# Optimization experiments

Measured on AMD Instinct MI355X. Metric: run time of the kernel, lower is better.

## Reference

```python
import jax, jax.numpy as jnp
import numpy as np

LOG2E = 1.4426950408889634
NUM_HEADS = 12

def fake_quant_sym8(x):
    # per-tensor symmetric int8 fake-quant (QuantStub with MovingAverageMinMax,
    # symmetric, qint8 [-128,127]); dynamic scale from current amax, STE.
    scale = jnp.maximum(jnp.max(jnp.abs(x)) / 127.0, 1e-8)
    q = jnp.clip(jnp.round(x / scale), -128.0, 127.0) * scale
    return x + jax.lax.stop_gradient(q - x)

def integer_approx_softmax(x):
    # ITA-style integer-approximated softmax: exp(x) = 2^(x*log2e),
    # split into integer/fractional parts, 2^f approximated piecewise-linearly
    # as (1 + f) for f in [0,1) (hardware shift-add friendly), then normalize.
    z = x * LOG2E
    z = z - jnp.max(z, axis=-1, keepdims=True)  # z <= 0, numerically stable
    zi = jnp.floor(z)
    zf = z - zi
    p = jnp.exp2(zi) * (1.0 + zf)
    return p / jnp.sum(p, axis=-1, keepdims=True)

def setup_inputs() -> dict:
    key = jax.random.key(0)
    ks = jax.random.split(key, 5)
    B, N, E, P = 8, 1024, 768, 768
    s = 0.02  # typical init scale for linear weights
    return {
        "x":  jax.random.normal(ks[0], (B, N, E), jnp.float32),
        "Wq": jax.random.normal(ks[1], (E, P), jnp.float32) * s,
        "bq": jnp.zeros((P,), jnp.float32),
        "Wk": jax.random.normal(ks[2], (E, P), jnp.float32) * s,
        "bk": jnp.zeros((P,), jnp.float32),
        "Wv": jax.random.normal(ks[3], (E, P), jnp.float32) * s,
        "bv": jnp.zeros((P,), jnp.float32),
        "Wo": jax.random.normal(ks[4], (P, E), jnp.float32) * s,
        "bo": jnp.zeros((E,), jnp.float32),
    }

def reference(x, Wq, bq, Wk, bk, Wv, bv, Wo, bo):
    B, N, E = x.shape
    H = NUM_HEADS
    D = Wq.shape[1] // H  # head_dim = proj_dim // num_heads
    xq = fake_quant_sym8(x)
    # projections -> [B, H, N, D]
    Q = (xq @ Wq + bq).reshape(B, N, H, D).transpose(0, 2, 1, 3)
    K = (xq @ Wk + bk).reshape(B, N, H, D).transpose(0, 2, 1, 3)
    V = (xq @ Wv + bv).reshape(B, N, H, D).transpose(0, 2, 1, 3)
    # NOTE: no 1/sqrt(D) scaling -- the torch module applies none (ITA absorbs
    # scaling into the quantization parameters).
    logits = jnp.einsum('bhnd,bhmd->bhnm', Q, K)
    attn = integer_approx_softmax(logits)
    ctx = jnp.einsum('bhnm,bhmd->bhnd', attn, V)
    ctx = ctx.transpose(0, 2, 1, 3).reshape(B, N, H * D)
    return ctx @ Wo + bo
```

## Files before the change

kernel.cpp:

```cpp
#include <hip/hip_runtime.h>


typedef unsigned short u16;
typedef __attribute__((ext_vector_type(8))) short short8;
typedef __attribute__((ext_vector_type(8))) _Float16 half8;
typedef __attribute__((ext_vector_type(4))) float f32x4;

#define LOG2E_F 1.4426950408889634f

static __device__ __forceinline__ half8 s2h(short8 s) {
  union { short8 s; half8 h; } u; u.s = s; return u.h;
}
static __device__ __forceinline__ f32x4 mfma16(short8 a, short8 b, f32x4 c) {
  return __builtin_amdgcn_mfma_f32_16x16x32_f16(s2h(a), s2h(b), c, 0, 0, 0);
}
static __device__ __forceinline__ u16 f2h(float f) {
  union { _Float16 h; u16 u; } v; v.h = (_Float16)f; return v.u;
}
static __device__ __forceinline__ void gload16(const void* g, void* l) {
  __builtin_amdgcn_global_load_lds(
      (const __attribute__((address_space(1))) void*)g,
      (__attribute__((address_space(3))) void*)l, 16, 0, 0);
}

__global__ __launch_bounds__(256) void amax_part_kernel(
    const float4* __restrict__ x, float* __restrict__ part, int n4) {
  float m = 0.f;
  int i = blockIdx.x * 256 + threadIdx.x;
  const int stride = gridDim.x * 256;
  for (; i < n4; i += stride) {
    float4 v = x[i];
    m = fmaxf(m, fmaxf(fmaxf(fabsf(v.x), fabsf(v.y)),
                       fmaxf(fabsf(v.z), fabsf(v.w))));
  }
  #pragma unroll
  for (int o = 1; o < 64; o <<= 1) m = fmaxf(m, __shfl_xor(m, o));
  __shared__ float sw[4];
  if ((threadIdx.x & 63) == 0) sw[threadIdx.x >> 6] = m;
  __syncthreads();
  if (threadIdx.x == 0)
    part[blockIdx.x] = fmaxf(fmaxf(sw[0], sw[1]), fmaxf(sw[2], sw[3]));
}

__global__ __launch_bounds__(256) void amax_fin_kernel(
    const float* __restrict__ part, double* __restrict__ dsc,
    float* __restrict__ dscf) {
  const int t = threadIdx.x;
  float m = fmaxf(fmaxf(part[t], part[t + 256]),
                  fmaxf(part[t + 512], part[t + 768]));
  #pragma unroll
  for (int o = 1; o < 64; o <<= 1) m = fmaxf(m, __shfl_xor(m, o));
  __shared__ float sw[4];
  if ((t & 63) == 0) sw[t >> 6] = m;
  __syncthreads();
  if (t == 0) {
    double sd = (double)(fmaxf(fmaxf(sw[0], sw[1]), fmaxf(sw[2], sw[3]))) / 127.0;
    if (sd < 1e-8) sd = 1e-8;
    dsc[0] = sd;
    dsc[1] = 1.0 / sd;
    dscf[0] = (float)sd;
  }
}

__global__ __launch_bounds__(256) void quant_kernel(
    const float4* __restrict__ x, u16* __restrict__ xq,
    const double* __restrict__ dsc, int n4) {
  const double rinv = dsc[1];
  int i = blockIdx.x * 256 + threadIdx.x;
  const int stride = gridDim.x * 256;
  for (; i < n4; i += stride) {
    float4 v = x[i];
    ushort4 u;
    u.x = f2h((float)fmin(fmax(rint((double)v.x * rinv), -128.0), 127.0));
    u.y = f2h((float)fmin(fmax(rint((double)v.y * rinv), -128.0), 127.0));
    u.z = f2h((float)fmin(fmax(rint((double)v.z * rinv), -128.0), 127.0));
    u.w = f2h((float)fmin(fmax(rint((double)v.w * rinv), -128.0), 127.0));
    *(ushort4*)&xq[(size_t)i * 4] = u;
  }
}

__global__ __launch_bounds__(256) void prep_weights_kernel(
    const float* __restrict__ Wq, const float* __restrict__ Wk,
    const float* __restrict__ Wv, const float* __restrict__ Wo,
    const float* __restrict__ bq, const float* __restrict__ bk,
    const float* __restrict__ bv,
    u16* __restrict__ Wcat, u16* __restrict__ Wot, float* __restrict__ bcat) {
  __shared__ float t[64][65];
  const int m = blockIdx.y;
  const float* src = (m == 0) ? Wq : (m == 1) ? Wk : (m == 2) ? Wv : Wo;
  u16* dst = (m == 3) ? Wot : (Wcat + (size_t)m * 768 * 768);
  const int tile = blockIdx.x;
  const int r0 = (tile / 12) * 64, c0 = (tile - (tile / 12) * 12) * 64;
  const int i = threadIdx.x >> 6, j = threadIdx.x & 63;
  #pragma unroll
  for (int it = 0; it < 16; ++it) {
    const int row = it * 4 + i;
    t[row][j] = src[(size_t)(r0 + row) * 768 + c0 + j];
  }
  __syncthreads();
  #pragma unroll
  for (int it = 0; it < 16; ++it) {
    const int row = it * 4 + i;
    dst[(size_t)(c0 + row) * 768 + r0 + j] = f2h(t[j][row]);
  }
  if (blockIdx.x == 0 && m == 0) {
    for (int k = threadIdx.x; k < 768; k += 256) {
      bcat[k] = bq[k];
      bcat[k + 768] = bk[k];
      bcat[k + 1536] = bv[k];
    }
  }
}

template <int MODE>
__global__ __launch_bounds__(256, 4) void gemm128(
    const u16* __restrict__ A, const u16* __restrict__ Bt,
    const float* __restrict__ bias, const float* __restrict__ scale_p,
    u16* __restrict__ Oq, u16* __restrict__ Ok, u16* __restrict__ Ovt,
    float* __restrict__ Of) {
  __shared__ u16 S[4][4608];
  const int K = 768, nk = 24;
  const int tid = threadIdx.x;
  const int w = tid >> 6, l = tid & 63;
  const int l15 = l & 15, lk = l >> 4;
  const int wr = w >> 1, wc = w & 1;
  const int bid = blockIdx.x;
  const int g = bid & 7, li = bid >> 3;
  const int tn = li >> 3, tm = g * 8 + (li & 7);
  f32x4 acc[4][4] = {};
  const int rA = tid >> 2;
  const int c8 = (tid & 3) * 8;
  const u16* gA = A + (size_t)(tm * 128 + rA) * K + c8;
  const u16* gB = Bt + (size_t)(tn * 128 + rA) * K + c8;
  {
    char* lA = (char*)S[0] + w * 1024;
    char* lB = (char*)S[2] + w * 1024;
    gload16(gA, lA);
    gload16(gA + (size_t)64 * K, lA + 4096);
    gload16(gB, lB);
    gload16(gB + (size_t)64 * K, lB + 4096);
  }
  __syncthreads();
  for (int kt = 0; kt < nk; ++kt) {
    const int buf = kt & 1;
    if (kt + 1 < nk) {
      const int k0 = (kt + 1) * 32;
      char* lA = (char*)S[buf ^ 1] + w * 1024;
      char* lB = (char*)S[2 + (buf ^ 1)] + w * 1024;
      gload16(gA + k0, lA);
      gload16(gA + k0 + (size_t)64 * K, lA + 4096);
      gload16(gB + k0, lB);
      gload16(gB + k0 + (size_t)64 * K, lB + 4096);
    }
    short8 af[4], bf[4];
    #pragma unroll
    for (int mi = 0; mi < 4; ++mi)
      af[mi] = *(const short8*)&S[buf][(wr * 64 + mi * 16 + l15) * 32 + lk * 8];
    #pragma unroll
    for (int ni = 0; ni < 4; ++ni)
      bf[ni] = *(const short8*)&S[2 + buf][(wc * 64 + ni * 16 + l15) * 32 + lk * 8];
    #pragma unroll
    for (int mi = 0; mi < 4; ++mi)
      #pragma unroll
      for (int ni = 0; ni < 4; ++ni)
        acc[mi][ni] = mfma16(af[mi], bf[ni], acc[mi][ni]);
    __syncthreads();
  }

  if (MODE == 1) {
    #pragma unroll
    for (int mi = 0; mi < 4; ++mi)
      #pragma unroll
      for (int ni = 0; ni < 4; ++ni)
        #pragma unroll
        for (int j = 0; j < 4; ++j) {
          const int gm = tm * 128 + wr * 64 + mi * 16 + lk * 4 + j;
          const int c = tn * 128 + wc * 64 + ni * 16 + l15;
          Of[(size_t)gm * 768 + c] = acc[mi][ni][j] + bias[c];
        }
    return;
  }

  __syncthreads();
  const float s = *scale_p;
  const int seg = tn / 6;
  const int h = (tn - seg * 6) * 2 + wc;
  u16* esc = &S[w][0];
  #pragma unroll
  for (int mi = 0; mi < 4; ++mi) {
    #pragma unroll
    for (int ni = 0; ni < 4; ++ni) {
      #pragma unroll
      for (int j = 0; j < 4; ++j) {
        const float v = acc[mi][ni][j] * s + bias[tn * 128 + wc * 64 + ni * 16 + l15];
        const int row = mi * 16 + lk * 4 + j;
        const int col = ni * 16 + l15;
        if (seg < 2) esc[row * 72 + col] = f2h(v);
        else         esc[col * 72 + row] = f2h(v);
      }
    }
  }
  asm volatile("s_waitcnt lgkmcnt(0)" ::: "memory");
  const int n0 = tm * 128 + wr * 64;
  const int b = n0 >> 10, nn = n0 & 1023;
  u16* outp = (seg == 0) ? Oq : (seg == 1) ? Ok : Ovt;
  #pragma unroll
  for (int it = 0; it < 8; ++it) {
    const int r = it * 8 + (l >> 3);
    const int cc = (l & 7) * 8;
    short8 vv = *(const short8*)&esc[r * 72 + cc];
    size_t o;
    if (seg < 2)
      o = (((size_t)b * 12 + h) * 1024 + nn + r) * 64 + cc;
    else
      o = (((size_t)b * 12 + h) * 64 + r) * 1024 + nn + cc;
    *(short8*)&outp[o] = vv;
  }
}

__global__ __launch_bounds__(512, 4) void attn_kernel(
    const u16* __restrict__ Q, const u16* __restrict__ K,
    const u16* __restrict__ Vt, u16* __restrict__ ctx) {
  __shared__ u16 Ks[2][64 * 64];
  __shared__ u16 Vs[2][64 * 64];
  __shared__ u16 Pw[8][16 * 40];
  const int bh = blockIdx.x, qt = blockIdx.y;
  const int b = bh / 12, h = bh - b * 12;
  const int tid = threadIdx.x;
  const int w = tid >> 6, l = tid & 63;
  const int l15 = l & 15, lk = l >> 4;
  const int xr = l15 & 7;

  const size_t qoff = ((size_t)bh * 1024 + qt * 128 + w * 16 + l15) * 64 + lk * 8;
  const short8 qa0 = *(const short8*)(Q + qoff);
  const short8 qa1 = *(const short8*)(Q + qoff + 32);

  const int srow = w * 8 + (l >> 3);
  const int schunk = ((l & 7) ^ ((l >> 3) & 7)) * 8;
  const u16* Kg = K + ((size_t)bh * 1024 + srow) * 64 + schunk;
  const u16* Vg = Vt + ((size_t)bh * 64 + srow) * 1024 + schunk;
  u16* const ksd[2] = {&Ks[0][w * 512], &Ks[1][w * 512]};
  u16* const vsd[2] = {&Vs[0][w * 512], &Vs[1][w * 512]};

  f32x4 mx = {-3e38f, -3e38f, -3e38f, -3e38f};
  gload16(Kg, ksd[0]);
  __syncthreads();
  for (int kt = 0; kt < 16; ++kt) {
    const int buf = kt & 1;
    if (kt < 15) gload16(Kg + (size_t)(kt + 1) * 4096, ksd[buf ^ 1]);
    const u16* kb = Ks[buf];
    #pragma unroll
    for (int ks = 0; ks < 4; ++ks) {
      short8 k0 = *(const short8*)&kb[(ks * 16 + l15) * 64 + ((lk ^ xr) * 8)];
      short8 k1 = *(const short8*)&kb[(ks * 16 + l15) * 64 + (((lk + 4) ^ xr) * 8)];
      f32x4 sv = {0.f, 0.f, 0.f, 0.f};
      sv = mfma16(qa0, k0, sv);
      sv = mfma16(qa1, k1, sv);
      #pragma unroll
      for (int j = 0; j < 4; ++j) mx[j] = fmaxf(mx[j], sv[j]);
    }
    __syncthreads();
  }
  #pragma unroll
  for (int o = 1; o < 16; o <<= 1) {
    #pragma unroll
    for (int j = 0; j < 4; ++j) mx[j] = fmaxf(mx[j], __shfl_xor(mx[j], o));
  }
  f32x4 mz;
  #pragma unroll
  for (int j = 0; j < 4; ++j) mz[j] = mx[j] * LOG2E_F;

  f32x4 sum = {0.f, 0.f, 0.f, 0.f};
  f32x4 pv[4] = {};
  u16* const pw = Pw[w];
  gload16(Kg, ksd[0]);
  gload16(Vg, vsd[0]);
  __syncthreads();
  for (int kt = 0; kt < 16; ++kt) {
    const int buf = kt & 1;
    if (kt < 15) {
      gload16(Kg + (size_t)(kt + 1) * 4096, ksd[buf ^ 1]);
      gload16(Vg + (size_t)(kt + 1) * 64, vsd[buf ^ 1]);
    }
    const u16* kb = Ks[buf];
    const u16* vb = Vs[buf];
    #pragma unroll
    for (int ko = 0; ko < 2; ++ko) {
      #pragma unroll
      for (int ks2 = 0; ks2 < 2; ++ks2) {
        const int ks = ko * 2 + ks2;
        short8 k0 = *(const short8*)&kb[(ks * 16 + l15) * 64 + ((lk ^ xr) * 8)];
        short8 k1 = *(const short8*)&kb[(ks * 16 + l15) * 64 + (((lk + 4) ^ xr) * 8)];
        f32x4 sv = {0.f, 0.f, 0.f, 0.f};
        sv = mfma16(qa0, k0, sv);
        sv = mfma16(qa1, k1, sv);
        #pragma unroll
        for (int j = 0; j < 4; ++j) {
          float z = sv[j] * LOG2E_F;
          float zz = z - mz[j];
          float zi = floorf(zz);
          float p = ldexpf(1.0f + (zz - zi), (int)zi);
          sum[j] += p;
          pw[(lk * 4 + j) * 40 + ks2 * 16 + l15] = f2h(p);
        }
      }
      asm volatile("s_waitcnt lgkmcnt(0)" ::: "memory");
      short8 pa = *(const short8*)&pw[l15 * 40 + lk * 8];
      #pragma unroll
      for (int dt = 0; dt < 4; ++dt) {
        short8 vv = *(const short8*)&vb[(dt * 16 + l15) * 64 +
                                        (((lk + 4 * ko) ^ xr) * 8)];
        pv[dt] = mfma16(pa, vv, pv[dt]);
      }
    }
    __syncthreads();
  }
  #pragma unroll
  for (int o = 1; o < 16; o <<= 1) {
    #pragma unroll
    for (int j = 0; j < 4; ++j) sum[j] += __shfl_xor(sum[j], o);
  }
  const int nrow = qt * 128 + w * 16 + lk * 4;
  #pragma unroll
  for (int dt = 0; dt < 4; ++dt) {
    #pragma unroll
    for (int j = 0; j < 4; ++j) {
      float v = pv[dt][j] / sum[j];
      ctx[((size_t)b * 1024 + nrow + j) * 768 + h * 64 + dt * 16 + l15] = f2h(v);
    }
  }
}

extern "C" void kernel_launch(void* const* d_in, const int* in_sizes, int n_in,
                              void* d_out, int out_size, void* d_ws, size_t ws_size,
                              hipStream_t stream) {
  const float* x  = (const float*)d_in[0];
  const float* Wq = (const float*)d_in[1];
  const float* bq = (const float*)d_in[2];
  const float* Wk = (const float*)d_in[3];
  const float* bk = (const float*)d_in[4];
  const float* Wv = (const float*)d_in[5];
  const float* bv = (const float*)d_in[6];
  const float* Wo = (const float*)d_in[7];
  const float* bo = (const float*)d_in[8];
  float* out = (float*)d_out;

  char* ws = (char*)d_ws;
  float* part  = (float*)ws;
  double* dsc  = (double*)(ws + 4096);
  float* dscf  = (float*)(ws + 4112);
  float* bcat  = (float*)(ws + 8192);
  size_t off = 8192 + 16384;
  const size_t WB = (size_t)768 * 768;
  const size_t XB = (size_t)8192 * 768;
  u16* xq   = (u16*)(ws + off); off += XB * 2;
  u16* Wcat = (u16*)(ws + off); off += 3 * WB * 2;
  u16* Wot  = (u16*)(ws + off); off += WB * 2;
  u16* Qb   = (u16*)(ws + off); off += XB * 2;
  u16* Kb   = (u16*)(ws + off); off += XB * 2;
  u16* Vtb  = (u16*)(ws + off); off += XB * 2;
  u16* ctx  = xq;
  (void)ws_size; (void)in_sizes; (void)n_in; (void)out_size;

  const int n4 = (8 * 1024 * 768) / 4;
  amax_part_kernel<<<1024, 256, 0, stream>>>((const float4*)x, part, n4);
  amax_fin_kernel<<<1, 256, 0, stream>>>(part, dsc, dscf);
  quant_kernel<<<2048, 256, 0, stream>>>((const float4*)x, xq, dsc, n4);
  prep_weights_kernel<<<dim3(144, 4), 256, 0, stream>>>(
      Wq, Wk, Wv, Wo, bq, bk, bv, Wcat, Wot, bcat);
  gemm128<0><<<1152, 256, 0, stream>>>(xq, Wcat, bcat, dscf,
                                       Qb, Kb, Vtb, nullptr);
  attn_kernel<<<dim3(96, 8), 512, 0, stream>>>(Qb, Kb, Vtb, ctx);
  gemm128<1><<<384, 256, 0, stream>>>(ctx, Wot, bo, nullptr,
                                      nullptr, nullptr, nullptr, out);
}
```

Baseline: 150.7 us.

## Load K and V fragments directly from global memory instead of LDS staging

Removes the double-buffered shared-memory staging of K and V tiles and the per-tile block barriers in both attention passes. Each wave now reads its MFMA operands straight from global memory, depending on L1/L2 caching for reuse across the 8 waves of a block. This drops the LDS traffic and __syncthreads stalls, but every wave issues redundant global loads and loses the cooperative async prefetch, so load latency is exposed unless occupancy hides it.

```diff
diff --git a/kernel.cpp b/kernel.cpp
--- a/kernel.cpp
+++ b/kernel.cpp
@@ -221,45 +221,31 @@
 __global__ __launch_bounds__(512, 4) void attn_kernel(
     const u16* __restrict__ Q, const u16* __restrict__ K,
     const u16* __restrict__ Vt, u16* __restrict__ ctx) {
-  __shared__ u16 Ks[2][64 * 64];
-  __shared__ u16 Vs[2][64 * 64];
   __shared__ u16 Pw[8][16 * 40];
   const int bh = blockIdx.x, qt = blockIdx.y;
   const int b = bh / 12, h = bh - b * 12;
   const int tid = threadIdx.x;
   const int w = tid >> 6, l = tid & 63;
   const int l15 = l & 15, lk = l >> 4;
-  const int xr = l15 & 7;
 
   const size_t qoff = ((size_t)bh * 1024 + qt * 128 + w * 16 + l15) * 64 + lk * 8;
   const short8 qa0 = *(const short8*)(Q + qoff);
   const short8 qa1 = *(const short8*)(Q + qoff + 32);
 
-  const int srow = w * 8 + (l >> 3);
-  const int schunk = ((l & 7) ^ ((l >> 3) & 7)) * 8;
-  const u16* Kg = K + ((size_t)bh * 1024 + srow) * 64 + schunk;
-  const u16* Vg = Vt + ((size_t)bh * 64 + srow) * 1024 + schunk;
-  u16* const ksd[2] = {&Ks[0][w * 512], &Ks[1][w * 512]};
-  u16* const vsd[2] = {&Vs[0][w * 512], &Vs[1][w * 512]};
+  const u16* Kb = K + (size_t)bh * 65536 + (size_t)l15 * 64 + lk * 8;
+  const u16* Vb = Vt + (size_t)bh * 65536 + (size_t)l15 * 1024 + lk * 8;
 
   f32x4 mx = {-3e38f, -3e38f, -3e38f, -3e38f};
-  gload16(Kg, ksd[0]);
-  __syncthreads();
-  for (int kt = 0; kt < 16; ++kt) {
-    const int buf = kt & 1;
-    if (kt < 15) gload16(Kg + (size_t)(kt + 1) * 4096, ksd[buf ^ 1]);
-    const u16* kb = Ks[buf];
-    #pragma unroll
-    for (int ks = 0; ks < 4; ++ks) {
-      short8 k0 = *(const short8*)&kb[(ks * 16 + l15) * 64 + ((lk ^ xr) * 8)];
-      short8 k1 = *(const short8*)&kb[(ks * 16 + l15) * 64 + (((lk + 4) ^ xr) * 8)];
-      f32x4 sv = {0.f, 0.f, 0.f, 0.f};
-      sv = mfma16(qa0, k0, sv);
-      sv = mfma16(qa1, k1, sv);
-      #pragma unroll
-      for (int j = 0; j < 4; ++j) mx[j] = fmaxf(mx[j], sv[j]);
-    }
-    __syncthreads();
+  #pragma unroll 4
+  for (int kb16 = 0; kb16 < 64; ++kb16) {
+    const u16* kp = Kb + (size_t)kb16 * 1024;
+    short8 k0 = *(const short8*)kp;
+    short8 k1 = *(const short8*)(kp + 32);
+    f32x4 sv = {0.f, 0.f, 0.f, 0.f};
+    sv = mfma16(qa0, k0, sv);
+    sv = mfma16(qa1, k1, sv);
+    #pragma unroll
+    for (int j = 0; j < 4; ++j) mx[j] = fmaxf(mx[j], sv[j]);
   }
   #pragma unroll
   for (int o = 1; o < 16; o <<= 1) {
@@ -273,24 +259,19 @@
   f32x4 sum = {0.f, 0.f, 0.f, 0.f};
   f32x4 pv[4] = {};
   u16* const pw = Pw[w];
-  gload16(Kg, ksd[0]);
-  gload16(Vg, vsd[0]);
-  __syncthreads();
   for (int kt = 0; kt < 16; ++kt) {
-    const int buf = kt & 1;
-    if (kt < 15) {
-      gload16(Kg + (size_t)(kt + 1) * 4096, ksd[buf ^ 1]);
-      gload16(Vg + (size_t)(kt + 1) * 64, vsd[buf ^ 1]);
-    }
-    const u16* kb = Ks[buf];
-    const u16* vb = Vs[buf];
     #pragma unroll
     for (int ko = 0; ko < 2; ++ko) {
+      short8 vv[4];
+      #pragma unroll
+      for (int dt = 0; dt < 4; ++dt)
+        vv[dt] = *(const short8*)(Vb + (size_t)dt * 16384 + kt * 64 + ko * 32);
       #pragma unroll
       for (int ks2 = 0; ks2 < 2; ++ks2) {
-        const int ks = ko * 2 + ks2;
-        short8 k0 = *(const short8*)&kb[(ks * 16 + l15) * 64 + ((lk ^ xr) * 8)];
-        short8 k1 = *(const short8*)&kb[(ks * 16 + l15) * 64 + (((lk + 4) ^ xr) * 8)];
+        const int kb16 = kt * 4 + ko * 2 + ks2;
+        const u16* kp = Kb + (size_t)kb16 * 1024;
+        short8 k0 = *(const short8*)kp;
+        short8 k1 = *(const short8*)(kp + 32);
         f32x4 sv = {0.f, 0.f, 0.f, 0.f};
         sv = mfma16(qa0, k0, sv);
         sv = mfma16(qa1, k1, sv);
@@ -307,13 +288,9 @@
       asm volatile("s_waitcnt lgkmcnt(0)" ::: "memory");
       short8 pa = *(const short8*)&pw[l15 * 40 + lk * 8];
       #pragma unroll
-      for (int dt = 0; dt < 4; ++dt) {
-        short8 vv = *(const short8*)&vb[(dt * 16 + l15) * 64 +
-                                        (((lk + 4 * ko) ^ xr) * 8)];
-        pv[dt] = mfma16(pa, vv, pv[dt]);
-      }
-    }
-    __syncthreads();
+      for (int dt = 0; dt < 4; ++dt)
+        pv[dt] = mfma16(pa, vv[dt], pv[dt]);
+    }
   }
   #pragma unroll
   for (int o = 1; o < 16; o <<= 1) {
```

Result: slower. 338.9 us (+124.9%).

## Process two 16-row query fragments per wave to reuse K/V tiles

Applied to the files above, without the earlier changes.

Each wave now handles 32 query rows (two MFMA row fragments) instead of 16, so each block covers 256 queries and the grid's query dimension halves. Every K and V fragment read from LDS, and every tile loaded from global memory, now feeds twice as many MFMAs, which cuts global and LDS traffic per query. In exchange each thread holds more registers (doubled Q fragments, accumulators, max and sum), which may lower occupancy. Fewer blocks (384) also means less parallelism across the GPU's compute units.

```diff
diff --git a/kernel.cpp b/kernel.cpp
--- a/kernel.cpp
+++ b/kernel.cpp
@@ -223,7 +223,7 @@
     const u16* __restrict__ Vt, u16* __restrict__ ctx) {
   __shared__ u16 Ks[2][64 * 64];
   __shared__ u16 Vs[2][64 * 64];
-  __shared__ u16 Pw[8][16 * 40];
+  __shared__ u16 Pw[8][32 * 40];
   const int bh = blockIdx.x, qt = blockIdx.y;
   const int b = bh / 12, h = bh - b * 12;
   const int tid = threadIdx.x;
@@ -231,18 +231,27 @@
   const int l15 = l & 15, lk = l >> 4;
   const int xr = l15 & 7;
 
-  const size_t qoff = ((size_t)bh * 1024 + qt * 128 + w * 16 + l15) * 64 + lk * 8;
-  const short8 qa0 = *(const short8*)(Q + qoff);
-  const short8 qa1 = *(const short8*)(Q + qoff + 32);
-
-  const int srow = w * 8 + (l >> 3);
-  const int schunk = ((l & 7) ^ ((l >> 3) & 7)) * 8;
+  short8 qa[2][2];
+  #pragma unroll
+  for (int rf = 0; rf < 2; ++rf) {
+    const size_t qoff =
+        ((size_t)bh * 1024 + qt * 256 + w * 32 + rf * 16 + l15) * 64 + lk * 8;
+    qa[rf][0] = *(const short8*)(Q + qoff);
+    qa[rf][1] = *(const short8*)(Q + qoff + 32);
+  }
+
+  const int srow = tid >> 3;
+  const int schunk = ((l & 7) ^ (srow & 7)) * 8;
   const u16* Kg = K + ((size_t)bh * 1024 + srow) * 64 + schunk;
   const u16* Vg = Vt + ((size_t)bh * 64 + srow) * 1024 + schunk;
   u16* const ksd[2] = {&Ks[0][w * 512], &Ks[1][w * 512]};
   u16* const vsd[2] = {&Vs[0][w * 512], &Vs[1][w * 512]};
 
-  f32x4 mx = {-3e38f, -3e38f, -3e38f, -3e38f};
+  f32x4 mx[2];
+  #pragma unroll
+  for (int rf = 0; rf < 2; ++rf)
+    #pragma unroll
+    for (int j = 0; j < 4; ++j) mx[rf][j] = -3e38f;
   gload16(Kg, ksd[0]);
   __syncthreads();
   for (int kt = 0; kt < 16; ++kt) {
@@ -253,25 +262,32 @@
     for (int ks = 0; ks < 4; ++ks) {
       short8 k0 = *(const short8*)&kb[(ks * 16 + l15) * 64 + ((lk ^ xr) * 8)];
       short8 k1 = *(const short8*)&kb[(ks * 16 + l15) * 64 + (((lk + 4) ^ xr) * 8)];
-      f32x4 sv = {0.f, 0.f, 0.f, 0.f};
-      sv = mfma16(qa0, k0, sv);
-      sv = mfma16(qa1, k1, sv);
-      #pragma unroll
-      for (int j = 0; j < 4; ++j) mx[j] = fmaxf(mx[j], sv[j]);
+      #pragma unroll
+      for (int rf = 0; rf < 2; ++rf) {
+        f32x4 sv = {0.f, 0.f, 0.f, 0.f};
+        sv = mfma16(qa[rf][0], k0, sv);
+        sv = mfma16(qa[rf][1], k1, sv);
+        #pragma unroll
+        for (int j = 0; j < 4; ++j) mx[rf][j] = fmaxf(mx[rf][j], sv[j]);
+      }
     }
     __syncthreads();
   }
-  #pragma unroll
-  for (int o = 1; o < 16; o <<= 1) {
-    #pragma unroll
-    for (int j = 0; j < 4; ++j) mx[j] = fmaxf(mx[j], __shfl_xor(mx[j], o));
-  }
-  f32x4 mz;
-  #pragma unroll
-  for (int j = 0; j < 4; ++j) mz[j] = mx[j] * LOG2E_F;
-
-  f32x4 sum = {0.f, 0.f, 0.f, 0.f};
-  f32x4 pv[4] = {};
+  f32x4 mz[2];
+  #pragma unroll
+  for (int rf = 0; rf < 2; ++rf) {
+    #pragma unroll
+    for (int o = 1; o < 16; o <<= 1) {
+      #pragma unroll
+      for (int j = 0; j < 4; ++j)
+        mx[rf][j] = fmaxf(mx[rf][j], __shfl_xor(mx[rf][j], o));
+    }
+    #pragma unroll
+    for (int j = 0; j < 4; ++j) mz[rf][j] = mx[rf][j] * LOG2E_F;
+  }
+
+  f32x4 sum[2] = {};
+  f32x4 pv[2][4] = {};
   u16* const pw = Pw[w];
   gload16(Kg, ksd[0]);
   gload16(Vg, vsd[0]);
@@ -291,42 +307,51 @@
         const int ks = ko * 2 + ks2;
         short8 k0 = *(const short8*)&kb[(ks * 16 + l15) * 64 + ((lk ^ xr) * 8)];
         short8 k1 = *(const short8*)&kb[(ks * 16 + l15) * 64 + (((lk + 4) ^ xr) * 8)];
-        f32x4 sv = {0.f, 0.f, 0.f, 0.f};
-        sv = mfma16(qa0, k0, sv);
-        sv = mfma16(qa1, k1, sv);
         #pragma unroll
-        for (int j = 0; j < 4; ++j) {
-          float z = sv[j] * LOG2E_F;
-          float zz = z - mz[j];
-          float zi = floorf(zz);
-          float p = ldexpf(1.0f + (zz - zi), (int)zi);
-          sum[j] += p;
-          pw[(lk * 4 + j) * 40 + ks2 * 16 + l15] = f2h(p);
+        for (int rf = 0; rf < 2; ++rf) {
+          f32x4 sv = {0.f, 0.f, 0.f, 0.f};
+          sv = mfma16(qa[rf][0], k0, sv);
+          sv = mfma16(qa[rf][1], k1, sv);
+          #pragma unroll
+          for (int j = 0; j < 4; ++j) {
+            float z = sv[j] * LOG2E_F;
+            float zz = z - mz[rf][j];
+            float zi = floorf(zz);
+            float p = ldexpf(1.0f + (zz - zi), (int)zi);
+            sum[rf][j] += p;
+            pw[(rf * 16 + lk * 4 + j) * 40 + ks2 * 16 + l15] = f2h(p);
+          }
         }
       }
       asm volatile("s_waitcnt lgkmcnt(0)" ::: "memory");
-      short8 pa = *(const short8*)&pw[l15 * 40 + lk * 8];
+      short8 pa0 = *(const short8*)&pw[l15 * 40 + lk * 8];
+      short8 pa1 = *(const short8*)&pw[(16 + l15) * 40 + lk * 8];
       #pragma unroll
       for (int dt = 0; dt < 4; ++dt) {
         short8 vv = *(const short8*)&vb[(dt * 16 + l15) * 64 +
                                         (((lk + 4 * ko) ^ xr) * 8)];
-        pv[dt] = mfma16(pa, vv, pv[dt]);
+        pv[0][dt] = mfma16(pa0, vv, pv[0][dt]);
+        pv[1][dt] = mfma16(pa1, vv, pv[1][dt]);
       }
     }
     __syncthreads();
   }
   #pragma unroll
-  for (int o = 1; o < 16; o <<= 1) {
-    #pragma unroll
-    for (int j = 0; j < 4; ++j) sum[j] += __shfl_xor(sum[j], o);
-  }
-  const int nrow = qt * 128 + w * 16 + lk * 4;
-  #pragma unroll
-  for (int dt = 0; dt < 4; ++dt) {
-    #pragma unroll
-    for (int j = 0; j < 4; ++j) {
-      float v = pv[dt][j] / sum[j];
-      ctx[((size_t)b * 1024 + nrow + j) * 768 + h * 64 + dt * 16 + l15] = f2h(v);
+  for (int rf = 0; rf < 2; ++rf) {
+    #pragma unroll
+    for (int o = 1; o < 16; o <<= 1) {
+      #pragma unroll
+      for (int j = 0; j < 4; ++j) sum[rf][j] += __shfl_xor(sum[rf][j], o);
+    }
+    const int nrow = qt * 256 + w * 32 + rf * 16 + lk * 4;
+    #pragma unroll
+    for (int dt = 0; dt < 4; ++dt) {
+      #pragma unroll
+      for (int j = 0; j < 4; ++j) {
+        float v = pv[rf][dt][j] / sum[rf][j];
+        ctx[((size_t)b * 1024 + nrow + j) * 768 + h * 64 + dt * 16 + l15] =
+            f2h(v);
+      }
     }
   }
 }
@@ -370,7 +395,7 @@
       Wq, Wk, Wv, Wo, bq, bk, bv, Wcat, Wot, bcat);
   gemm128<0><<<1152, 256, 0, stream>>>(xq, Wcat, bcat, dscf,
                                        Qb, Kb, Vtb, nullptr);
-  attn_kernel<<<dim3(96, 8), 512, 0, stream>>>(Qb, Kb, Vtb, ctx);
+  attn_kernel<<<dim3(96, 4), 512, 0, stream>>>(Qb, Kb, Vtb, ctx);
   gemm128<1><<<384, 256, 0, stream>>>(ctx, Wot, bo, nullptr,
                                       nullptr, nullptr, nullptr, out);
 }
```

Measured after the change: 148.7 us. No clear change (-1.3%).
